# Optimization experiments

Hardware: AMD Instinct MI355X
Metric: run time of the kernel (lower is better)

The kernel has to match this reference:

```python
import jax, jax.numpy as jnp
import numpy as np

B, NQ, NKV = 2, 2048, 2048
QUERY_DIM = 1024
CONTEXT_DIM = 1024
HEADS = 16
DIM_HEAD = 64
INNER = HEADS * DIM_HEAD
SCALE = DIM_HEAD ** -0.5


def setup_inputs() -> dict:
    key = jax.random.key(0)
    ks = jax.random.split(key, 9)
    x = jax.random.normal(ks[0], (B, NQ, QUERY_DIM), dtype=jnp.float32)
    context = jax.random.normal(ks[1], (B, NKV, CONTEXT_DIM), dtype=jnp.float32)
    tgt_mask = jax.random.randint(ks[2], (B, 1, NQ, NKV), 0, 2, dtype=jnp.int32)
    src_mask = jax.random.randint(ks[3], (B, 1, NKV), 0, 2) > 0  # bool [b,1,j]
    w = 0.02
    Wq = jax.random.normal(ks[4], (INNER, QUERY_DIM), dtype=jnp.float32) * w
    Wk = jax.random.normal(ks[5], (INNER, CONTEXT_DIM), dtype=jnp.float32) * w
    Wv = jax.random.normal(ks[6], (INNER, CONTEXT_DIM), dtype=jnp.float32) * w
    Wo = jax.random.normal(ks[7], (QUERY_DIM, INNER), dtype=jnp.float32) * w
    bo = jax.random.normal(ks[8], (QUERY_DIM,), dtype=jnp.float32) * w
    return {"x": x, "context": context, "tgt_mask": tgt_mask, "src_mask": src_mask,
            "Wq": Wq, "Wk": Wk, "Wv": Wv, "Wo": Wo, "bo": bo}


def reference(x, context, tgt_mask, src_mask, Wq, Wk, Wv, Wo, bo):
    b, nq, _ = x.shape
    nkv = context.shape[1]
    # Linear projections (torch Linear: y = x @ W.T), split into heads: b n (h d) -> b h n d
    q = jnp.einsum('bnc,ec->bne', x, Wq).reshape(b, nq, HEADS, DIM_HEAD).transpose(0, 2, 1, 3)
    k = jnp.einsum('bmc,ec->bme', context, Wk).reshape(b, nkv, HEADS, DIM_HEAD).transpose(0, 2, 1, 3)
    v = jnp.einsum('bmc,ec->bme', context, Wv).reshape(b, nkv, HEADS, DIM_HEAD).transpose(0, 2, 1, 3)
    sim = jnp.einsum('bhid,bhjd->bhij', q, k) * SCALE
    neg = -jnp.finfo(sim.dtype).max
    sim = jnp.where(tgt_mask == 0, neg, sim)                 # tgt_mask [b,1,i,j]
    sim = jnp.where(src_mask[:, None, :], sim, neg)          # src_mask [b,1,j] -> [b,1,1,j]
    attn = jax.nn.softmax(sim, axis=-1)
    out = jnp.einsum('bhij,bhjd->bhid', attn, v)
    out = out.transpose(0, 2, 1, 3).reshape(b, nq, INNER)    # b h n d -> b n (h d)
    return jnp.einsum('bne,oe->bno', out, Wo) + bo           # dropout=0 at inference
```

## Files before the change

### kernel.cpp

```cpp
#include <hip/hip_runtime.h>

typedef short short8 __attribute__((ext_vector_type(8)));
typedef float f32x4 __attribute__((ext_vector_type(4)));
typedef float f32x16 __attribute__((ext_vector_type(16)));
typedef unsigned u32x4 __attribute__((ext_vector_type(4)));

#define GLOAD_LDS(src, dst) \
  __builtin_amdgcn_global_load_lds((const __attribute__((address_space(1))) void*)(src), \
                                   (__attribute__((address_space(3))) void*)(dst), 16, 0, 0)

__device__ __forceinline__ unsigned short f2b(float f){
  __bf16 h = (__bf16)f;
  return __builtin_bit_cast(unsigned short, h);
}
__device__ __forceinline__ unsigned pk2(float a, float b){
  unsigned r;
  asm("v_cvt_pk_bf16_f32 %0, %1, %2" : "=v"(r) : "v"(a), "v"(b));
  return r;
}
__device__ __forceinline__ float fexp2(float x){
  return __builtin_amdgcn_exp2f(x);
}
__device__ __forceinline__ float b2f(unsigned short u){
  union { unsigned u; float f; } cv;
  cv.u = ((unsigned)u) << 16;
  return cv.f;
}

__global__ __launch_bounds__(256) void prep(const float* __restrict__ x, const float* __restrict__ ctx,
    const float* __restrict__ wq, const float* __restrict__ wk, const float* __restrict__ wv,
    const float* __restrict__ wo, const int* __restrict__ tgt, const void* __restrict__ srcm,
    unsigned short* __restrict__ xb, unsigned short* __restrict__ cb, unsigned short* __restrict__ wqb,
    unsigned short* __restrict__ wkvb, unsigned short* __restrict__ wob,
    unsigned* __restrict__ mpT2){
  const int blk = blockIdx.x;
  if (blk < 2048){
    for (int i = blk * 256 + threadIdx.x; i < 3145728; i += 2048 * 256){
      const float* src; unsigned short* dst; int so, doff;
      if (i < 1048576)      { src = x;   dst = xb;   so = i;           doff = so; }
      else if (i < 2097152) { src = ctx; dst = cb;   so = i - 1048576; doff = so; }
      else if (i < 2359296) { src = wq;  dst = wqb;  so = i - 2097152; doff = so; }
      else if (i < 2621440) { src = wk;  dst = wkvb; so = i - 2359296; doff = so; }
      else if (i < 2883584) { src = wv;  dst = wkvb; so = i - 2621440; doff = so + 262144; }
      else                  { src = wo;  dst = wob;  so = i - 2883584; doff = so; }
      const float4 v = reinterpret_cast<const float4*>(src)[so];
      ushort4 o;
      o.x = f2b(v.x); o.y = f2b(v.y); o.z = f2b(v.z); o.w = f2b(v.w);
      reinterpret_cast<ushort4*>(dst)[doff] = o;
    }
  } else {
    const int t = (blk - 2048) * 4 + (threadIdx.x >> 6);
    const int lane = threadIdx.x & 63;
    const int bb = t >> 10, it = (t >> 5) & 31, jt = t & 31;
    const unsigned dw = ((const unsigned*)srcm)[((bb * 2048 + jt * 64) >> 2) + (lane & 15)];
    const bool u8mode = __ballot(dw > 1u) != 0ull;
    bool sbit;
    if (u8mode) sbit = ((const unsigned char*)srcm)[bb * 2048 + jt * 64 + lane] != 0;
    else        sbit = ((const int*)srcm)[bb * 2048 + jt * 64 + lane] != 0;
    unsigned long long xv = 0ull;
    const int* tg = tgt + ((size_t)(bb * 2048 + it * 64)) * 2048 + jt * 64 + lane;
    #pragma unroll
    for (int rb = 0; rb < 64; rb += 8){
      int v[8];
      #pragma unroll
      for (int r = 0; r < 8; r++)
        v[r] = tg[(size_t)(rb + r) * 2048];
      #pragma unroll
      for (int r = 0; r < 8; r++){
        const unsigned long long wbits = __ballot(sbit && (v[r] != 0));
        xv = (lane == rb + r) ? wbits : xv;
      }
    }
    const unsigned long long A0 = 0x00000000FFFFFFFFull, A1 = 0x0000FFFF0000FFFFull,
                             A2 = 0x00FF00FF00FF00FFull, A3 = 0x0F0F0F0F0F0F0F0Full,
                             A4 = 0x3333333333333333ull, A5 = 0x5555555555555555ull;
#define TRSTEP(K, A) { \
    unsigned long long y = __shfl_xor(xv, K); \
    xv = (lane & (K)) ? (((y >> (K)) & (A)) | (xv & ~(A))) \
                      : ((xv & (A)) | ((y & (A)) << (K))); }
    TRSTEP(32, A0) TRSTEP(16, A1) TRSTEP(8, A2) TRSTEP(4, A3) TRSTEP(2, A4) TRSTEP(1, A5)
#undef TRSTEP
    unsigned* dst = mpT2 + (((size_t)bb * 32 + jt) * 64 + it * 2) * 64 + lane;
    dst[0]  = (unsigned)xv;
    dst[64] = (unsigned)(xv >> 32);
  }
}

#define G_DECLS \
  const int tid = threadIdx.x; \
  const int lane = tid & 63, wid = tid >> 6; \
  const int l15 = lane & 15, l4 = lane >> 4; \
  const int wm = wid >> 1, wn = wid & 1; \
  __shared__ unsigned short lA[3][128 * 32]; \
  __shared__ unsigned short lB[3][128 * 32]; \
  f32x4 acc[4][4] = {}; \
  const int r0 = tid >> 2, q0 = tid & 3; \
  const int r1 = (tid + 256) >> 2; \
  const unsigned short* a0p = A  + (size_t)(m0 + r0) * 1024 + q0 * 8; \
  const unsigned short* a1p = A  + (size_t)(m0 + r1) * 1024 + q0 * 8; \
  const unsigned short* b0p = Bw + (size_t)(n0 + r0) * 1024 + q0 * 8; \
  const unsigned short* b1p = Bw + (size_t)(n0 + r1) * 1024 + q0 * 8; \
  const int d0 = (wid * 64) * 8, d1 = (wid * 64 + 256) * 8;

#define G_STAGE(K0, BUF) { \
    GLOAD_LDS(a0p + (K0), &lA[BUF][d0]); \
    GLOAD_LDS(a1p + (K0), &lA[BUF][d1]); \
    GLOAD_LDS(b0p + (K0), &lB[BUF][d0]); \
    GLOAD_LDS(b1p + (K0), &lB[BUF][d1]); }

#define GCOMPUTE(BR) { \
  short8 af[4], bf[4]; \
  _Pragma("unroll") for (int m = 0; m < 4; m++) \
    af[m] = *reinterpret_cast<const short8*>(&lA[BR][(wm * 64 + m * 16 + l15) * 32 + l4 * 8]); \
  _Pragma("unroll") for (int n = 0; n < 4; n++) \
    bf[n] = *reinterpret_cast<const short8*>(&lB[BR][(wn * 64 + n * 16 + l15) * 32 + l4 * 8]); \
  _Pragma("unroll") for (int m = 0; m < 4; m++) \
    _Pragma("unroll") for (int n = 0; n < 4; n++) \
      acc[m][n] = __builtin_amdgcn_mfma_f32_16x16x32_bf16(af[m], bf[n], acc[m][n], 0, 0, 0); \
}

#define GITER(T, BR, BS, VM) { \
  asm volatile("s_waitcnt vmcnt(" #VM ")\n\ts_barrier" ::: "memory"); \
  if ((T) < 30) G_STAGE(((T) + 2) * 32, BS) \
  GCOMPUTE(BR) \
}

#define G_LOOP \
  G_STAGE(0, 0) \
  G_STAGE(32, 1) \
  for (int u = 0; u < 30; u += 3){ \
    GITER(u, 0, 2, 4) \
    GITER(u + 1, 1, 0, 4) \
    GITER(u + 2, 2, 1, 4) \
  } \
  GITER(30, 0, 2, 4) \
  GITER(31, 1, 0, 0)

__global__ __launch_bounds__(256, 3) void gemm_qkv(const unsigned short* __restrict__ xb,
                                                const unsigned short* __restrict__ cbuf,
                                                const unsigned short* __restrict__ wqb,
                                                const unsigned short* __restrict__ wkvb,
                                                unsigned short* __restrict__ qws,
                                                unsigned short* __restrict__ kws,
                                                unsigned short* __restrict__ vtw){
  const int f = blockIdx.x;
  const unsigned short *A, *Bw;
  int m0, n0, mode;
  if (f < 256){
    const int xcd = f & 7, idx = f >> 3;
    A = xb;   Bw = wqb;
    m0 = (xcd * 4 + (idx >> 3)) * 128;  n0 = (idx & 7) * 128;  mode = 0;
  } else {
    const int g = f - 256;
    const int xcd = g & 7, idx = g >> 3;
    A = cbuf; Bw = wkvb;
    m0 = (xcd * 4 + (idx >> 4)) * 128;  n0 = (idx & 15) * 128; mode = 1;
  }
  G_DECLS
  G_LOOP

  const int eb = n0 + wn * 64;
  const int mb = m0 + wm * 64 + l4 * 4;
  #pragma unroll
  for (int n = 0; n < 4; n++){
    const int e = eb + n * 16 + l15;
    #pragma unroll
    for (int m = 0; m < 4; m++){
      const int mm = mb + m * 16;
      if (mode == 0){
        const int h = e >> 6, d = e & 63;
        #pragma unroll
        for (int r = 0; r < 4; r++){
          const int row = mm + r, b = row >> 11, nn = row & 2047;
          qws[(((size_t)b * 16 + h) * 2048 + nn) * 64 + d] = f2b(acc[m][n][r] * 0.18033688011112042f);
        }
      } else {
        if (e < 1024){
          const int h = e >> 6, d = e & 63;
          #pragma unroll
          for (int r = 0; r < 4; r++){
            const int row = mm + r, b = row >> 11, nn = row & 2047;
            kws[(((size_t)b * 16 + h) * 2048 + nn) * 64 + d] = f2b(acc[m][n][r]);
          }
        } else {
          const int ee = e - 1024, h = ee >> 6, d = ee & 63;
          const int b = mm >> 11, nn = mm & 2047;
          ushort4 pk;
          pk.x = f2b(acc[m][n][0]); pk.y = f2b(acc[m][n][1]);
          pk.z = f2b(acc[m][n][2]); pk.w = f2b(acc[m][n][3]);
          *reinterpret_cast<ushort4*>(&vtw[(((size_t)b * 16 + h) * 64 + d) * 2048 + nn]) = pk;
        }
      }
    }
  }
}

__global__ __launch_bounds__(256, 3) void gemm_o(const unsigned short* __restrict__ A,
                                              const unsigned short* __restrict__ Bw,
                                              float* __restrict__ fout,
                                              const float* __restrict__ bias){
  const int f = blockIdx.x;
  const int xcd = f & 7, idx = f >> 3;
  const int m0 = (xcd * 4 + (idx >> 3)) * 128, n0 = (idx & 7) * 128;
  G_DECLS
  G_LOOP

  const int eb = n0 + wn * 64;
  const int mb = m0 + wm * 64 + l4 * 4;
  #pragma unroll
  for (int n = 0; n < 4; n++){
    const int e = eb + n * 16 + l15;
    const float bv = bias[e];
    #pragma unroll
    for (int m = 0; m < 4; m++){
      const int mm = mb + m * 16;
      #pragma unroll
      for (int r = 0; r < 4; r++)
        fout[(size_t)(mm + r) * 1024 + e] = acc[m][n][r] + bv;
    }
  }
}

#define A_STAGE(T, BUF) { \
    const int jj = jbase + (T) * 64; \
    GLOAD_LDS(kb + (size_t)(jj + sr0) * 64 + sc0 * 8, &lK[BUF][dk0]); \
    GLOAD_LDS(kb + (size_t)(jj + sr1) * 64 + sc1 * 8, &lK[BUF][dk1]); \
    GLOAD_LDS(vb + (size_t)sr0 * 2048 + jj + sc0 * 8, &lV[BUF][dk0]); \
    GLOAD_LDS(vb + (size_t)sr1 * 2048 + jj + sc1 * 8, &lV[BUF][dk1]); }

#define A_COMPUTE(BR, T) { \
  const char* kbase = (const char*)lK[BR]; \
  f32x16 st0 = {}, st1 = {}; \
  __builtin_amdgcn_s_setprio(1); \
  _Pragma("unroll") for (int ks = 0; ks < 4; ks++){ \
    const short8 a0 = *reinterpret_cast<const short8*>(kbase + (((l31) * 128 + ks * 32 + hi * 16) ^ sw)); \
    st0 = __builtin_amdgcn_mfma_f32_32x32x16_bf16(a0, qf[ks], st0, 0, 0, 0); \
  } \
  _Pragma("unroll") for (int ks = 0; ks < 4; ks++){ \
    const short8 a1 = *reinterpret_cast<const short8*>(kbase + (((l31 + 32) * 128 + ks * 32 + hi * 16) ^ sw)); \
    st1 = __builtin_amdgcn_mfma_f32_32x32x16_bf16(a1, qf[ks], st1, 0, 0, 0); \
  } \
  __builtin_amdgcn_s_setprio(0); \
  const unsigned* mt = mt0 + (size_t)(T) * 4096; \
  _Pragma("unroll") for (int r = 0; r < 16; r++){ \
    const int dj = (r & 3) + 8 * (r >> 2); \
    const unsigned long long mk0 = (unsigned long long)mt[dj] | ((unsigned long long)mt[dj + 4] << 32); \
    const unsigned long long mk1 = (unsigned long long)mt[dj + 32] | ((unsigned long long)mt[dj + 36] << 32); \
    float v0, v1; \
    asm("v_cndmask_b32 %0, %1, %2, %3" : "=v"(v0) : "v"(negv), "v"((float)st0[r]), "s"(mk0)); \
    asm("v_cndmask_b32 %0, %1, %2, %3" : "=v"(v1) : "v"(negv), "v"((float)st1[r]), "s"(mk1)); \
    st0[r] = fexp2(v0); \
    st1[r] = fexp2(v1); \
  } \
  float s8[8]; \
  _Pragma("unroll") for (int i = 0; i < 8; i++) \
    s8[i] = (st0[i] + st0[i + 8]) + (st1[i] + st1[i + 8]); \
  l_i += ((s8[0] + s8[1]) + (s8[2] + s8[3])) + ((s8[4] + s8[5]) + (s8[6] + s8[7])); \
  const char* vbase = (const char*)lV[BR]; \
  _Pragma("unroll") for (int ks = 0; ks < 4; ks++){ \
    unsigned A0, B0, A1, B1; \
    if (ks < 2){ \
      A0 = pk2(st0[8 * ks + 0], st0[8 * ks + 1]); \
      B0 = pk2(st0[8 * ks + 2], st0[8 * ks + 3]); \
      A1 = pk2(st0[8 * ks + 4], st0[8 * ks + 5]); \
      B1 = pk2(st0[8 * ks + 6], st0[8 * ks + 7]); \
    } else { \
      A0 = pk2(st1[8 * (ks - 2) + 0], st1[8 * (ks - 2) + 1]); \
      B0 = pk2(st1[8 * (ks - 2) + 2], st1[8 * (ks - 2) + 3]); \
      A1 = pk2(st1[8 * (ks - 2) + 4], st1[8 * (ks - 2) + 5]); \
      B1 = pk2(st1[8 * (ks - 2) + 6], st1[8 * (ks - 2) + 7]); \
    } \
    asm("v_permlane32_swap_b32 %0, %1" : "+v"(A0), "+v"(A1)); \
    asm("v_permlane32_swap_b32 %0, %1" : "+v"(B0), "+v"(B1)); \
    const short8 pf = __builtin_bit_cast(short8, (u32x4){A0, B0, A1, B1}); \
    __builtin_amdgcn_s_setprio(1); \
    const short8 va0 = *reinterpret_cast<const short8*>(vbase + (((l31) * 128 + ks * 32 + hi * 16) ^ sw)); \
    o0_ = __builtin_amdgcn_mfma_f32_32x32x16_bf16(va0, pf, o0_, 0, 0, 0); \
    const short8 va1 = *reinterpret_cast<const short8*>(vbase + (((l31 + 32) * 128 + ks * 32 + hi * 16) ^ sw)); \
    o1_ = __builtin_amdgcn_mfma_f32_32x32x16_bf16(va1, pf, o1_, 0, 0, 0); \
    __builtin_amdgcn_s_setprio(0); \
  } \
}

__global__ __launch_bounds__(256, 4) void attn(const unsigned short* __restrict__ qw,
                                            const unsigned short* __restrict__ kw,
                                            const unsigned short* __restrict__ vtw,
                                            const unsigned* __restrict__ mpT2,
                                            unsigned short* __restrict__ opb,
                                            float* __restrict__ lsum){
  const int f = blockIdx.x;
  const int xcd = f & 7, slot = f >> 3;
  const int bh = xcd * 4 + (slot & 3);
  const int r2 = slot >> 2;
  const int qtile = r2 >> 1, kvh = r2 & 1;
  const int b = bh >> 4;
  const int qbase = qtile * 128;
  const int jbase = kvh * 1024;
  const int tid = threadIdx.x, wid = tid >> 6, lane = tid & 63;
  const int l31 = lane & 31, hi = lane >> 5;
  __shared__ unsigned short lK[2][64 * 64];
  __shared__ unsigned short lV[2][64 * 64];

  const int qrow = qbase + wid * 32 + l31;
  const unsigned short* qp = qw + ((size_t)bh * 2048 + qrow) * 64 + hi * 8;
  short8 qf[4];
  #pragma unroll
  for (int ks = 0; ks < 4; ks++)
    qf[ks] = *reinterpret_cast<const short8*>(qp + ks * 16);

  const int sr0 = tid >> 3,          sc0 = (tid & 7) ^ (sr0 & 7);
  const int sr1 = (tid + 256) >> 3,  sc1 = ((tid + 256) & 7) ^ (sr1 & 7);
  const unsigned short* kb = kw  + (size_t)bh * 2048 * 64;
  const unsigned short* vb = vtw + (size_t)bh * 64 * 2048;
  const int dk0 = (wid * 64) * 8, dk1 = (wid * 64 + 256) * 8;

  const int widu = __builtin_amdgcn_readfirstlane(wid);
  const int qw32 = qtile * 4 + widu;
  const unsigned* mt0 = mpT2 + (((size_t)b * 32 + kvh * 16) * 64 + qw32) * 64;

  float l_i = 0.f;
  f32x16 o0_ = {}, o1_ = {};
  const int sw = (l31 & 7) << 4;
  const float negv = -3.0e38f;

  A_STAGE(0, 0)
  __syncthreads();

  int cb_ = 0;
  for (int t = 0; t < 16; t++){
    if (t < 15) A_STAGE(t + 1, cb_ ^ 1)
    A_COMPUTE(cb_, t)
    if (t < 15) __syncthreads();
    cb_ ^= 1;
  }

  l_i += __shfl_xor(l_i, 32);
  const int row = wid * 32 + l31;
  const int pidx = (bh * 16 + qtile) * 2 + kvh;
  unsigned short* opr = opb + (size_t)pidx * 8192 + row * 64;
  #pragma unroll
  for (int rq = 0; rq < 4; rq++){
    uint2 w0, w1;
    w0.x = pk2(o0_[rq * 4 + 0], o0_[rq * 4 + 1]); w0.y = pk2(o0_[rq * 4 + 2], o0_[rq * 4 + 3]);
    w1.x = pk2(o1_[rq * 4 + 0], o1_[rq * 4 + 1]); w1.y = pk2(o1_[rq * 4 + 2], o1_[rq * 4 + 3]);
    *reinterpret_cast<uint2*>(opr + rq * 8 + hi * 4)      = w0;
    *reinterpret_cast<uint2*>(opr + 32 + rq * 8 + hi * 4) = w1;
  }
  if (!hi)
    lsum[pidx * 128 + row] = l_i;
}

__global__ __launch_bounds__(256) void combine(const unsigned short* __restrict__ opb,
                                               const float* __restrict__ lsum,
                                               unsigned short* __restrict__ ao){
  const int g = blockIdx.x;
  const int bh = g >> 4, qtile = g & 15;
  const int b = bh >> 4, h = bh & 15;
  const int row = threadIdx.x >> 1;
  const int dh = (threadIdx.x & 1) * 32;
  const float l = lsum[(g * 2 + 0) * 128 + row] + lsum[(g * 2 + 1) * 128 + row];
  const float inv = 1.f / l;
  const unsigned short* p0 = opb + ((size_t)(g * 2 + 0)) * 8192 + row * 64 + dh;
  const unsigned short* p1 = opb + ((size_t)(g * 2 + 1)) * 8192 + row * 64 + dh;
  unsigned short* o = ao + ((size_t)b * 2048 + qtile * 128 + row) * 1024 + h * 64 + dh;
  #pragma unroll
  for (int i = 0; i < 4; i++){
    short8 v0 = *reinterpret_cast<const short8*>(p0 + i * 8);
    short8 v1 = *reinterpret_cast<const short8*>(p1 + i * 8);
    ushort4 wa, wb;
    #pragma unroll
    for (int e = 0; e < 4; e++){
      ((unsigned short*)&wa)[e] = f2b((b2f((unsigned short)v0[e]) + b2f((unsigned short)v1[e])) * inv);
      ((unsigned short*)&wb)[e] = f2b((b2f((unsigned short)v0[e + 4]) + b2f((unsigned short)v1[e + 4])) * inv);
    }
    reinterpret_cast<ushort4*>(o)[i * 2]     = wa;
    reinterpret_cast<ushort4*>(o)[i * 2 + 1] = wb;
  }
}

extern "C" void kernel_launch(void* const* d_in, const int* in_sizes, int n_in,
                              void* d_out, int out_size, void* d_ws, size_t ws_size,
                              hipStream_t stream){
  const float* x   = (const float*)d_in[0];
  const float* ctx = (const float*)d_in[1];
  const int*   tgt = (const int*)d_in[2];
  const void*  src = d_in[3];
  const float* Wq  = (const float*)d_in[4];
  const float* Wk  = (const float*)d_in[5];
  const float* Wv  = (const float*)d_in[6];
  const float* Wo  = (const float*)d_in[7];
  const float* bo  = (const float*)d_in[8];
  float* out = (float*)d_out;

  char* w = (char*)d_ws;
  unsigned short* xb   = (unsigned short*)(w);
  unsigned short* cb   = (unsigned short*)(w + (8u << 20));
  unsigned short* wqb  = (unsigned short*)(w + (16u << 20));
  unsigned short* wkvb = (unsigned short*)(w + (18u << 20));
  unsigned short* wob  = (unsigned short*)(w + (22u << 20));
  unsigned short* qws  = (unsigned short*)(w + (24u << 20));
  unsigned short* kws  = (unsigned short*)(w + (32u << 20));
  unsigned short* vtw  = (unsigned short*)(w + (40u << 20));
  unsigned* mpT2       = (unsigned*)(w + (48u << 20));
  unsigned short* opb  = (unsigned short*)(w + (50u << 20));
  float* lsum = (float*)(w + (8u << 20));
  unsigned short* ao = (unsigned short*)(w);

  prep<<<2560, 256, 0, stream>>>(x, ctx, Wq, Wk, Wv, Wo, tgt, src,
                                 xb, cb, wqb, wkvb, wob, mpT2);
  gemm_qkv<<<768, 256, 0, stream>>>(xb, cb, wqb, wkvb, qws, kws, vtw);
  attn<<<1024, 256, 0, stream>>>(qws, kws, vtw, mpT2, opb, lsum);
  combine<<<512, 256, 0, stream>>>(opb, lsum, ao);
  gemm_o<<<256, 256, 0, stream>>>(ao, wob, out, bo);
}
```

Baseline: 135.5 us.

## Fuse split-KV combine into attention kernel via last-arriver atomic counter

Removes the separate combine kernel launch. Each attention block bumps a per-(head, q-tile) atomic counter after writing its partial output, and the second of the two KV-half blocks to finish merges both partials into the final bf16 attention output. A counter reset is added as an extra block in the prep kernel. This trades a kernel launch and its scheduling gap for a threadfence, an atomic and a tail of extra work in half the attention blocks.

```diff
diff --git a/kernel.cpp b/kernel.cpp
--- a/kernel.cpp
+++ b/kernel.cpp
@@ -32,8 +32,12 @@
     const float* __restrict__ wo, const int* __restrict__ tgt, const void* __restrict__ srcm,
     unsigned short* __restrict__ xb, unsigned short* __restrict__ cb, unsigned short* __restrict__ wqb,
     unsigned short* __restrict__ wkvb, unsigned short* __restrict__ wob,
-    unsigned* __restrict__ mpT2){
+    unsigned* __restrict__ mpT2, int* __restrict__ cnt){
   const int blk = blockIdx.x;
+  if (blk == 2560){
+    if (threadIdx.x < 256){ cnt[threadIdx.x] = 0; cnt[threadIdx.x + 256] = 0; }
+    return;
+  }
   if (blk < 2048){
     for (int i = blk * 256 + threadIdx.x; i < 3145728; i += 2048 * 256){
       const float* src; unsigned short* dst; int so, doff;
@@ -287,7 +291,9 @@
                                             const unsigned short* __restrict__ vtw,
                                             const unsigned* __restrict__ mpT2,
                                             unsigned short* __restrict__ opb,
-                                            float* __restrict__ lsum){
+                                            float* __restrict__ lsum,
+                                            unsigned short* __restrict__ ao,
+                                            int* __restrict__ cnt){
   const int f = blockIdx.x;
   const int xcd = f & 7, slot = f >> 3;
   const int bh = xcd * 4 + (slot & 3);
@@ -300,6 +306,7 @@
   const int l31 = lane & 31, hi = lane >> 5;
   __shared__ unsigned short lK[2][64 * 64];
   __shared__ unsigned short lV[2][64 * 64];
+  __shared__ int cflag;
 
   const int qrow = qbase + wid * 32 + l31;
   const unsigned short* qp = qw + ((size_t)bh * 2048 + qrow) * 64 + hi * 8;
@@ -348,33 +355,34 @@
   }
   if (!hi)
     lsum[pidx * 128 + row] = l_i;
-}
-
-__global__ __launch_bounds__(256) void combine(const unsigned short* __restrict__ opb,
-                                               const float* __restrict__ lsum,
-                                               unsigned short* __restrict__ ao){
-  const int g = blockIdx.x;
-  const int bh = g >> 4, qtile = g & 15;
-  const int b = bh >> 4, h = bh & 15;
-  const int row = threadIdx.x >> 1;
-  const int dh = (threadIdx.x & 1) * 32;
-  const float l = lsum[(g * 2 + 0) * 128 + row] + lsum[(g * 2 + 1) * 128 + row];
-  const float inv = 1.f / l;
-  const unsigned short* p0 = opb + ((size_t)(g * 2 + 0)) * 8192 + row * 64 + dh;
-  const unsigned short* p1 = opb + ((size_t)(g * 2 + 1)) * 8192 + row * 64 + dh;
-  unsigned short* o = ao + ((size_t)b * 2048 + qtile * 128 + row) * 1024 + h * 64 + dh;
-  #pragma unroll
-  for (int i = 0; i < 4; i++){
-    short8 v0 = *reinterpret_cast<const short8*>(p0 + i * 8);
-    short8 v1 = *reinterpret_cast<const short8*>(p1 + i * 8);
-    ushort4 wa, wb;
+
+  __threadfence();
+  if (tid == 0)
+    cflag = (atomicAdd(&cnt[bh * 16 + qtile], 1) == 1);
+  __syncthreads();
+  if (cflag){
+    __threadfence();
+    const int g = bh * 16 + qtile;
+    const int crow = tid >> 1;
+    const int dh = (tid & 1) * 32;
+    const float l = lsum[(g * 2 + 0) * 128 + crow] + lsum[(g * 2 + 1) * 128 + crow];
+    const float inv = 1.f / l;
+    const unsigned short* p0 = opb + ((size_t)(g * 2 + 0)) * 8192 + crow * 64 + dh;
+    const unsigned short* p1 = opb + ((size_t)(g * 2 + 1)) * 8192 + crow * 64 + dh;
+    unsigned short* o = ao + ((size_t)b * 2048 + qtile * 128 + crow) * 1024 + (bh & 15) * 64 + dh;
     #pragma unroll
-    for (int e = 0; e < 4; e++){
-      ((unsigned short*)&wa)[e] = f2b((b2f((unsigned short)v0[e]) + b2f((unsigned short)v1[e])) * inv);
-      ((unsigned short*)&wb)[e] = f2b((b2f((unsigned short)v0[e + 4]) + b2f((unsigned short)v1[e + 4])) * inv);
+    for (int i = 0; i < 4; i++){
+      short8 v0 = *reinterpret_cast<const short8*>(p0 + i * 8);
+      short8 v1 = *reinterpret_cast<const short8*>(p1 + i * 8);
+      ushort4 wa, wb;
+      #pragma unroll
+      for (int e = 0; e < 4; e++){
+        ((unsigned short*)&wa)[e] = f2b((b2f((unsigned short)v0[e]) + b2f((unsigned short)v1[e])) * inv);
+        ((unsigned short*)&wb)[e] = f2b((b2f((unsigned short)v0[e + 4]) + b2f((unsigned short)v1[e + 4])) * inv);
+      }
+      reinterpret_cast<ushort4*>(o)[i * 2]     = wa;
+      reinterpret_cast<ushort4*>(o)[i * 2 + 1] = wb;
     }
-    reinterpret_cast<ushort4*>(o)[i * 2]     = wa;
-    reinterpret_cast<ushort4*>(o)[i * 2 + 1] = wb;
   }
 }
 
@@ -403,13 +411,13 @@
   unsigned short* vtw  = (unsigned short*)(w + (40u << 20));
   unsigned* mpT2       = (unsigned*)(w + (48u << 20));
   unsigned short* opb  = (unsigned short*)(w + (50u << 20));
+  int* cnt             = (int*)(w + (66u << 20));
   float* lsum = (float*)(w + (8u << 20));
   unsigned short* ao = (unsigned short*)(w);
 
-  prep<<<2560, 256, 0, stream>>>(x, ctx, Wq, Wk, Wv, Wo, tgt, src,
-                                 xb, cb, wqb, wkvb, wob, mpT2);
+  prep<<<2561, 256, 0, stream>>>(x, ctx, Wq, Wk, Wv, Wo, tgt, src,
+                                 xb, cb, wqb, wkvb, wob, mpT2, cnt);
   gemm_qkv<<<768, 256, 0, stream>>>(xb, cb, wqb, wkvb, qws, kws, vtw);
-  attn<<<1024, 256, 0, stream>>>(qws, kws, vtw, mpT2, opb, lsum);
-  combine<<<512, 256, 0, stream>>>(opb, lsum, ao);
+  attn<<<1024, 256, 0, stream>>>(qws, kws, vtw, mpT2, opb, lsum, ao, cnt);
   gemm_o<<<256, 256, 0, stream>>>(ao, wob, out, bo);
 }
```

Measured after the change: 337.1 us. +148.8%, slower.
